# Performance work log

Measured on AMD Instinct MI355X. Metric: run time of the kernel, lower is better.

The kernel has to match this reference:

```python
import jax, jax.numpy as jnp
import numpy as np

N_NODES = 50000
N_EDGES = 800000
IN_DIM = 128
HID = 64
HEADS = 4
OUT_DIM = 64
NEG_SLOPE = 0.2


def setup_inputs() -> dict:
    key = jax.random.key(0)
    ks = jax.random.split(key, 12)
    x = jax.random.normal(ks[0], (N_NODES, IN_DIM), dtype=jnp.float32)
    edge_index = jax.random.randint(ks[1], (2, N_EDGES), 0, N_NODES, dtype=jnp.int64)
    s = 0.1
    # GATConv layer 1: in_dim -> hid per head, 4 heads, concat
    W1 = jax.random.normal(ks[2], (IN_DIM, HEADS * HID), dtype=jnp.float32) * s
    a_src1 = jax.random.normal(ks[3], (HEADS, HID), dtype=jnp.float32) * s
    a_dst1 = jax.random.normal(ks[4], (HEADS, HID), dtype=jnp.float32) * s
    b1 = jnp.zeros((HEADS * HID,), dtype=jnp.float32)
    # GATConv layer 2: hid*heads -> out_dim, 1 head
    W2 = jax.random.normal(ks[5], (HEADS * HID, OUT_DIM), dtype=jnp.float32) * s
    a_src2 = jax.random.normal(ks[6], (1, OUT_DIM), dtype=jnp.float32) * s
    a_dst2 = jax.random.normal(ks[7], (1, OUT_DIM), dtype=jnp.float32) * s
    b2 = jnp.zeros((OUT_DIM,), dtype=jnp.float32)
    # final linear out_dim -> 1
    fc_w = jax.random.normal(ks[8], (OUT_DIM, 1), dtype=jnp.float32) * s
    fc_b = jnp.zeros((1,), dtype=jnp.float32)
    return {"x": x, "edge_index": edge_index, "W1": W1, "a_src1": a_src1,
            "a_dst1": a_dst1, "b1": b1, "W2": W2, "a_src2": a_src2,
            "a_dst2": a_dst2, "b2": b2, "fc_w": fc_w, "fc_b": fc_b}


def _gat_layer(x, src, dst, W, a_src, a_dst, bias, heads, out_c):
    """PyG-style GATConv: gather, edge attention, segment softmax, scatter-sum."""
    n = x.shape[0]
    h = (x @ W).reshape(n, heads, out_c)                    # [N,H,C]
    alpha_s = jnp.sum(h * a_src, axis=-1)                   # [N,H]
    alpha_d = jnp.sum(h * a_dst, axis=-1)                   # [N,H]
    e = jax.nn.leaky_relu(alpha_s[src] + alpha_d[dst], NEG_SLOPE)  # [E,H]
    # segment softmax over incoming edges of each destination node
    m = jax.ops.segment_max(e, dst, num_segments=n)         # [N,H]
    ex = jnp.exp(e - m[dst])
    den = jax.ops.segment_sum(ex, dst, num_segments=n)      # [N,H]
    alpha = ex / (den[dst] + 1e-16)                         # [E,H]
    out = jax.ops.segment_sum(alpha[:, :, None] * h[src], dst, num_segments=n)
    return out.reshape(n, heads * out_c) + bias


def reference(x, edge_index, W1, a_src1, a_dst1, b1, W2, a_src2, a_dst2, b2, fc_w, fc_b):
    n = x.shape[0]
    # GATConv default add_self_loops=True
    loop = jnp.arange(n, dtype=edge_index.dtype)
    src = jnp.concatenate([edge_index[0], loop])
    dst = jnp.concatenate([edge_index[1], loop])
    h = _gat_layer(x, src, dst, W1, a_src1, a_dst1, b1, HEADS, HID)
    h = jax.nn.elu(h)
    h = _gat_layer(h, src, dst, W2, a_src2, a_dst2, b2, 1, OUT_DIM)
    return jnp.squeeze(h @ fc_w + fc_b)                      # [N]
```

## Files before the change

kernel.cpp:

```cpp
#include <hip/hip_runtime.h>

#define N_NODES 50000
#define N_EDGES 800000
#define E_TOT   850000
#define IN_DIM  128
#define HID     64
#define HEADS   4
#define C1      256
#define OUT_DIM 64
#define NEG_SLOPE 0.2f

#define CP_NODES   32
#define CP_BLOCKS  ((N_NODES + CP_NODES - 1) / CP_NODES)
#define COUNT_BLOCKS ((E_TOT + 255) / 256)
#define NB_SCAN ((N_NODES + 255) / 256)

typedef __attribute__((ext_vector_type(8))) short v8s;
typedef __attribute__((ext_vector_type(4))) float v4f;

__device__ __forceinline__ unsigned int bf16_rne(float f) {
    unsigned int u = __float_as_uint(f);
    return (u + 0x7FFFu + ((u >> 16) & 1u)) >> 16;
}
__device__ __forceinline__ unsigned int bf16_pack2(float a, float b) {
    return bf16_rne(a) | (bf16_rne(b) << 16);
}
__device__ __forceinline__ float bf16_lo(unsigned int u) { return __uint_as_float(u << 16); }
__device__ __forceinline__ float bf16_hi(unsigned int u) { return __uint_as_float(u & 0xFFFF0000u); }

__global__ __launch_bounds__(512) void prep_kernel(
    const float* __restrict__ W1, const float* __restrict__ a_src1,
    const float* __restrict__ a_dst1,
    const float* __restrict__ W2, const float* __restrict__ a_src2,
    const float* __restrict__ a_dst2, const float* __restrict__ b2,
    const float* __restrict__ fc_w, const float* __restrict__ fc_b,
    float* __restrict__ p_src, float* __restrict__ p_dst,
    float* __restrict__ v_s, float* __restrict__ v_d, float* __restrict__ v_z,
    float* __restrict__ cst, unsigned int* __restrict__ W1b)
{
    const int t = threadIdx.x;
    const int k = t >> 2, h = t & 3;
    const float* wrow = W1 + k * C1 + h * HID;
    const float* as = a_src1 + h * HID;
    const float* ad = a_dst1 + h * HID;
    float s = 0.f, d = 0.f;
    for (int c = 0; c < HID; c++) {
        float w = wrow[c];
        s = fmaf(w, as[c], s);
        d = fmaf(w, ad[c], d);
    }
    p_src[k * HEADS + h] = s;
    p_dst[k * HEADS + h] = d;

    if (t < C1) {
        const float* w2row = W2 + t * OUT_DIM;
        float vs = 0.f, vd = 0.f, vz = 0.f;
        for (int c = 0; c < OUT_DIM; c++) {
            float w = w2row[c];
            vs = fmaf(w, a_src2[c], vs);
            vd = fmaf(w, a_dst2[c], vd);
            vz = fmaf(w, fc_w[c], vz);
        }
        v_s[t] = vs; v_d[t] = vd; v_z[t] = vz;
    }
    if (t == 0) {
        float s2 = 0.f;
        for (int c = 0; c < OUT_DIM; c++) s2 = fmaf(b2[c], fc_w[c], s2);
        cst[0] = s2 + fc_b[0];
    }

    for (int idx = t; idx < 16384; idx += 512) {
        int i    = idx & 3;
        int lane = (idx >> 2) & 63;
        int kk   = (idx >> 8) & 3;
        int nt   = (idx >> 10) & 3;
        int hh   = idx >> 12;
        int k0 = kk * 32 + (lane >> 4) * 8 + i * 2;
        int c  = hh * 64 + nt * 16 + (lane & 15);
        W1b[idx] = bf16_pack2(W1[(size_t)k0 * C1 + c], W1[(size_t)(k0 + 1) * C1 + c]);
    }
}

__global__ __launch_bounds__(256) void convproj_count_kernel(
    const float* __restrict__ x, const float* __restrict__ p_src,
    const float* __restrict__ p_dst, const int* __restrict__ dst_a,
    float* __restrict__ as1, float* __restrict__ ad1,
    unsigned int* __restrict__ xb, int* __restrict__ deg)
{
    if (blockIdx.x >= CP_BLOCKS) {
        int j = (blockIdx.x - CP_BLOCKS) * 256 + threadIdx.x;
        if (j < E_TOT) {
            int d = (j < N_EDGES) ? dst_a[j] : (j - N_EDGES);
            atomicAdd(&deg[d], 1);
        }
        return;
    }
    __shared__ float ps[IN_DIM * HEADS];
    __shared__ float pd[IN_DIM * HEADS];
    const int t = threadIdx.x;
    for (int i = t; i < IN_DIM * HEADS; i += 256) { ps[i] = p_src[i]; pd[i] = p_dst[i]; }
    __syncthreads();
    const int wv   = t >> 6;
    const int lane = t & 63;
    float4 p0 = *(const float4*)(ps + (lane * 2) * HEADS);
    float4 p1 = *(const float4*)(ps + (lane * 2 + 1) * HEADS);
    float4 q0 = *(const float4*)(pd + (lane * 2) * HEADS);
    float4 q1 = *(const float4*)(pd + (lane * 2 + 1) * HEADS);
    const int nodeBase = blockIdx.x * CP_NODES + wv * 8;
    #pragma unroll
    for (int i = 0; i < 8; i++) {
        const int node = nodeBase + i;
        if (node >= N_NODES) break;
        float2 xv = *(const float2*)(x + (size_t)node * IN_DIM + lane * 2);
        xb[(size_t)node * 64 + lane] = bf16_pack2(xv.x, xv.y);
        float s0 = xv.x * p0.x + xv.y * p1.x;
        float s1 = xv.x * p0.y + xv.y * p1.y;
        float s2 = xv.x * p0.z + xv.y * p1.z;
        float s3 = xv.x * p0.w + xv.y * p1.w;
        float d0 = xv.x * q0.x + xv.y * q1.x;
        float d1 = xv.x * q0.y + xv.y * q1.y;
        float d2 = xv.x * q0.z + xv.y * q1.z;
        float d3 = xv.x * q0.w + xv.y * q1.w;
        #pragma unroll
        for (int off = 32; off; off >>= 1) {
            s0 += __shfl_down(s0, off, 64); s1 += __shfl_down(s1, off, 64);
            s2 += __shfl_down(s2, off, 64); s3 += __shfl_down(s3, off, 64);
            d0 += __shfl_down(d0, off, 64); d1 += __shfl_down(d1, off, 64);
            d2 += __shfl_down(d2, off, 64); d3 += __shfl_down(d3, off, 64);
        }
        if (lane == 0) {
            float4 sv = {s0, s1, s2, s3};
            float4 dv = {d0, d1, d2, d3};
            *(float4*)(as1 + node * 4) = sv;
            *(float4*)(ad1 + node * 4) = dv;
        }
    }
}

__global__ __launch_bounds__(256) void blocksum_kernel(
    const int* __restrict__ deg, int* __restrict__ bsum)
{
    __shared__ int ps[256];
    const int t = threadIdx.x;
    int i = blockIdx.x * 256 + t;
    ps[t] = (i < N_NODES) ? deg[i] : 0;
    __syncthreads();
    for (int off = 128; off; off >>= 1) {
        if (t < off) ps[t] += ps[t + off];
        __syncthreads();
    }
    if (t == 0) bsum[blockIdx.x] = ps[0];
}

__global__ __launch_bounds__(256) void scanbsum_kernel(
    const int* __restrict__ bsum, int* __restrict__ boff)
{
    __shared__ int ps[256];
    const int t = threadIdx.x;
    ps[t] = (t < NB_SCAN) ? bsum[t] : 0;
    __syncthreads();
    for (int off = 1; off < 256; off <<= 1) {
        int u = (t >= off) ? ps[t - off] : 0;
        __syncthreads();
        ps[t] += u;
        __syncthreads();
    }
    boff[t] = (t > 0) ? ps[t - 1] : 0;
}

__global__ __launch_bounds__(256) void expand_kernel(
    const int* __restrict__ deg, const int* __restrict__ boff,
    int* __restrict__ rowptr)
{
    __shared__ int ps[256];
    const int t = threadIdx.x;
    int i = blockIdx.x * 256 + t;
    int v = (i < N_NODES) ? deg[i] : 0;
    ps[t] = v;
    __syncthreads();
    for (int off = 1; off < 256; off <<= 1) {
        int u = (t >= off) ? ps[t - off] : 0;
        __syncthreads();
        ps[t] += u;
        __syncthreads();
    }
    if (i <= N_NODES) rowptr[i] = boff[blockIdx.x] + ps[t] - v;
}

__global__ void fillw_kernel(const int* __restrict__ src_a, const int* __restrict__ dst_a,
                             const int* __restrict__ rowptr, int* __restrict__ cursor,
                             const float* __restrict__ as1, const float* __restrict__ ad1,
                             int* __restrict__ srcSorted, float4* __restrict__ wS)
{
    int j = blockIdx.x * blockDim.x + threadIdx.x;
    if (j >= E_TOT) return;
    int s, d;
    if (j < N_EDGES) { s = src_a[j]; d = dst_a[j]; }
    else             { s = j - N_EDGES; d = s; }
    int pos = atomicAdd(&cursor[d], 1);
    int slot = rowptr[d] + pos;
    srcSorted[slot] = s;
    float4 A  = *(const float4*)(as1 + s * 4);
    float4 Dv = *(const float4*)(ad1 + d * 4);
    float a0 = A.x + Dv.x, a1 = A.y + Dv.y, a2 = A.z + Dv.z, a3 = A.w + Dv.w;
    a0 = a0 > 0.f ? a0 : NEG_SLOPE * a0;
    a1 = a1 > 0.f ? a1 : NEG_SLOPE * a1;
    a2 = a2 > 0.f ? a2 : NEG_SLOPE * a2;
    a3 = a3 > 0.f ? a3 : NEG_SLOPE * a3;
    float4 w = {__expf(a0), __expf(a1), __expf(a2), __expf(a3)};
    wS[slot] = w;
}

__global__ __launch_bounds__(256) void agg1x_kernel(
    const int* __restrict__ rowptr, const int* __restrict__ srcS,
    const float4* __restrict__ wS, const unsigned int* __restrict__ xb,
    unsigned int* __restrict__ xaggb)
{
    int gid  = blockIdx.x * blockDim.x + threadIdx.x;
    int n    = gid >> 6;
    int lane = threadIdx.x & 63;
    if (n >= N_NODES) return;
    const int e0 = rowptr[n], e1 = rowptr[n + 1];

    float2 acc0 = {0,0}, acc1 = {0,0}, acc2 = {0,0}, acc3 = {0,0};
    float den0 = 0, den1 = 0, den2 = 0, den3 = 0;
    int e = e0;
    for (; e + 4 <= e1; e += 4) {
        int s0 = srcS[e], s1 = srcS[e + 1], s2 = srcS[e + 2], s3 = srcS[e + 3];
        float4 W0 = wS[e],     W1 = wS[e + 1];
        float4 W2 = wS[e + 2], W3 = wS[e + 3];
        unsigned int xu0 = xb[(size_t)s0 * 64 + lane];
        unsigned int xu1 = xb[(size_t)s1 * 64 + lane];
        unsigned int xu2 = xb[(size_t)s2 * 64 + lane];
        unsigned int xu3 = xb[(size_t)s3 * 64 + lane];
        float a0 = bf16_lo(xu0), b0 = bf16_hi(xu0);
        float a1 = bf16_lo(xu1), b1 = bf16_hi(xu1);
        float a2 = bf16_lo(xu2), b2 = bf16_hi(xu2);
        float a3 = bf16_lo(xu3), b3 = bf16_hi(xu3);
        acc0.x = fmaf(W0.x, a0, acc0.x); acc0.y = fmaf(W0.x, b0, acc0.y);
        acc1.x = fmaf(W0.y, a0, acc1.x); acc1.y = fmaf(W0.y, b0, acc1.y);
        acc2.x = fmaf(W0.z, a0, acc2.x); acc2.y = fmaf(W0.z, b0, acc2.y);
        acc3.x = fmaf(W0.w, a0, acc3.x); acc3.y = fmaf(W0.w, b0, acc3.y);
        acc0.x = fmaf(W1.x, a1, acc0.x); acc0.y = fmaf(W1.x, b1, acc0.y);
        acc1.x = fmaf(W1.y, a1, acc1.x); acc1.y = fmaf(W1.y, b1, acc1.y);
        acc2.x = fmaf(W1.z, a1, acc2.x); acc2.y = fmaf(W1.z, b1, acc2.y);
        acc3.x = fmaf(W1.w, a1, acc3.x); acc3.y = fmaf(W1.w, b1, acc3.y);
        acc0.x = fmaf(W2.x, a2, acc0.x); acc0.y = fmaf(W2.x, b2, acc0.y);
        acc1.x = fmaf(W2.y, a2, acc1.x); acc1.y = fmaf(W2.y, b2, acc1.y);
        acc2.x = fmaf(W2.z, a2, acc2.x); acc2.y = fmaf(W2.z, b2, acc2.y);
        acc3.x = fmaf(W2.w, a2, acc3.x); acc3.y = fmaf(W2.w, b2, acc3.y);
        acc0.x = fmaf(W3.x, a3, acc0.x); acc0.y = fmaf(W3.x, b3, acc0.y);
        acc1.x = fmaf(W3.y, a3, acc1.x); acc1.y = fmaf(W3.y, b3, acc1.y);
        acc2.x = fmaf(W3.z, a3, acc2.x); acc2.y = fmaf(W3.z, b3, acc2.y);
        acc3.x = fmaf(W3.w, a3, acc3.x); acc3.y = fmaf(W3.w, b3, acc3.y);
        den0 += (W0.x + W1.x) + (W2.x + W3.x);
        den1 += (W0.y + W1.y) + (W2.y + W3.y);
        den2 += (W0.z + W1.z) + (W2.z + W3.z);
        den3 += (W0.w + W1.w) + (W2.w + W3.w);
    }
    for (; e < e1; e++) {
        int s = srcS[e];
        float4 W0 = wS[e];
        unsigned int xu = xb[(size_t)s * 64 + lane];
        float xa = bf16_lo(xu), xbv = bf16_hi(xu);
        acc0.x = fmaf(W0.x, xa, acc0.x); acc0.y = fmaf(W0.x, xbv, acc0.y);
        acc1.x = fmaf(W0.y, xa, acc1.x); acc1.y = fmaf(W0.y, xbv, acc1.y);
        acc2.x = fmaf(W0.z, xa, acc2.x); acc2.y = fmaf(W0.z, xbv, acc2.y);
        acc3.x = fmaf(W0.w, xa, acc3.x); acc3.y = fmaf(W0.w, xbv, acc3.y);
        den0 += W0.x; den1 += W0.y; den2 += W0.z; den3 += W0.w;
    }
    float i0 = 1.f / (den0 + 1e-16f), i1 = 1.f / (den1 + 1e-16f);
    float i2 = 1.f / (den2 + 1e-16f), i3 = 1.f / (den3 + 1e-16f);
    unsigned int* o = xaggb + (size_t)n * 256 + lane;
    o[0 * 64] = bf16_pack2(acc0.x * i0, acc0.y * i0);
    o[1 * 64] = bf16_pack2(acc1.x * i1, acc1.y * i1);
    o[2 * 64] = bf16_pack2(acc2.x * i2, acc2.y * i2);
    o[3 * 64] = bf16_pack2(acc3.x * i3, acc3.y * i3);
}

__global__ __launch_bounds__(256, 4) void mlp7_kernel(
    const unsigned int* __restrict__ xaggb,
    const unsigned int* __restrict__ W1b, const float* __restrict__ b1,
    const float* __restrict__ v_s, const float* __restrict__ v_d,
    const float* __restrict__ v_z,
    float2* __restrict__ az, float* __restrict__ ad2)
{
    __shared__ unsigned int xsh[16 * 260];
    __shared__ float pr[4 * 16 * 3];
    const int t = threadIdx.x;
    const int nodeBase = blockIdx.x * 16;
    const int h = t >> 6;
    const int lane = t & 63;

    {
        const unsigned int* gsrc = xaggb + (size_t)nodeBase * 256;
        #pragma unroll
        for (int i = 0; i < 4; i++) {
            int iu = i * 1024 + t * 4;
            uint4 v = *(const uint4*)(gsrc + iu);
            int n = iu >> 8, c = iu & 255;
            *(uint4*)(xsh + n * 260 + c) = v;
        }
    }
    __syncthreads();

    {
        const int m = lane & 15, quad = lane >> 4;
        const unsigned int* abase = xsh + m * 260 + h * 64 + quad * 4;
        v8s af0 = *(const v8s*)(abase + 0);
        v8s af1 = *(const v8s*)(abase + 16);
        v8s af2 = *(const v8s*)(abase + 32);
        v8s af3 = *(const v8s*)(abase + 48);

        float Sr[4] = {0,0,0,0}, Dr[4] = {0,0,0,0}, Zr[4] = {0,0,0,0};
        #pragma unroll
        for (int nt = 0; nt < 4; nt++) {
            const unsigned int* bbase = W1b + (size_t)(h * 16 + nt * 4) * 256 + lane * 4;
            v4f acc = {0.f, 0.f, 0.f, 0.f};
            acc = __builtin_amdgcn_mfma_f32_16x16x32_bf16(af0, *(const v8s*)(bbase + 0 * 256), acc, 0, 0, 0);
            acc = __builtin_amdgcn_mfma_f32_16x16x32_bf16(af1, *(const v8s*)(bbase + 1 * 256), acc, 0, 0, 0);
            acc = __builtin_amdgcn_mfma_f32_16x16x32_bf16(af2, *(const v8s*)(bbase + 2 * 256), acc, 0, 0, 0);
            acc = __builtin_amdgcn_mfma_f32_16x16x32_bf16(af3, *(const v8s*)(bbase + 3 * 256), acc, 0, 0, 0);
            const int c = h * 64 + nt * 16 + m;
            float bb = b1[c], vsc = v_s[c], vdc = v_d[c], vzc = v_z[c];
            #pragma unroll
            for (int r = 0; r < 4; r++) {
                float o = acc[r] + bb;
                o = o > 0.f ? o : __expf(o) - 1.f;
                Sr[r] = fmaf(o, vsc, Sr[r]);
                Dr[r] = fmaf(o, vdc, Dr[r]);
                Zr[r] = fmaf(o, vzc, Zr[r]);
            }
        }
        #pragma unroll
        for (int off = 8; off; off >>= 1) {
            #pragma unroll
            for (int r = 0; r < 4; r++) {
                Sr[r] += __shfl_down(Sr[r], off, 16);
                Dr[r] += __shfl_down(Dr[r], off, 16);
                Zr[r] += __shfl_down(Zr[r], off, 16);
            }
        }
        if (m == 0) {
            #pragma unroll
            for (int r = 0; r < 4; r++) {
                const int row = quad * 4 + r;
                pr[(h * 16 + row) * 3 + 0] = Sr[r];
                pr[(h * 16 + row) * 3 + 1] = Dr[r];
                pr[(h * 16 + row) * 3 + 2] = Zr[r];
            }
        }
    }
    __syncthreads();

    if (t < 16) {
        float s = 0.f, d = 0.f, z = 0.f;
        #pragma unroll
        for (int w = 0; w < 4; w++) {
            s += pr[(w * 16 + t) * 3 + 0];
            d += pr[(w * 16 + t) * 3 + 1];
            z += pr[(w * 16 + t) * 3 + 2];
        }
        const int node = nodeBase + t;
        float2 azv = {s, z};
        az[node]  = azv;
        ad2[node] = d;
    }
}

__global__ __launch_bounds__(256) void agg2z_kernel(
    const int* __restrict__ rowptr, const int* __restrict__ srcS,
    const float2* __restrict__ az, const float* __restrict__ ad2,
    const float* __restrict__ cst, float* __restrict__ out)
{
    int gid  = blockIdx.x * blockDim.x + threadIdx.x;
    int n    = gid >> 3;
    int sl   = threadIdx.x & 7;
    if (n >= N_NODES) return;
    const float adh = ad2[n];
    const int e0 = rowptr[n], e1 = rowptr[n + 1];

    float acc = 0.f, den = 0.f;
    for (int e = e0 + sl; e < e1; e += 8) {
        int s = srcS[e];
        float2 v = az[s];
        float a = v.x + adh;
        a = a > 0.f ? a : NEG_SLOPE * a;
        float w = __expf(a);
        acc = fmaf(w, v.y, acc);
        den += w;
    }
    #pragma unroll
    for (int off = 4; off; off >>= 1) {
        acc += __shfl_down(acc, off, 8);
        den += __shfl_down(den, off, 8);
    }
    if (sl == 0) out[n] = acc / (den + 1e-16f) + cst[0];
}

extern "C" void kernel_launch(void* const* d_in, const int* in_sizes, int n_in,
                              void* d_out, int out_size, void* d_ws, size_t ws_size,
                              hipStream_t stream)
{
    const float* x      = (const float*)d_in[0];
    const int*   ei     = (const int*)d_in[1];
    const float* W1     = (const float*)d_in[2];
    const float* a_src1 = (const float*)d_in[3];
    const float* a_dst1 = (const float*)d_in[4];
    const float* b1     = (const float*)d_in[5];
    const float* W2     = (const float*)d_in[6];
    const float* a_src2 = (const float*)d_in[7];
    const float* a_dst2 = (const float*)d_in[8];
    const float* b2     = (const float*)d_in[9];
    const float* fc_w   = (const float*)d_in[10];
    const float* fc_b   = (const float*)d_in[11];
    float* out = (float*)d_out;

    const int* srcA = ei;
    const int* dstA = ei + N_EDGES;

    float* ws = (float*)d_ws;
    size_t off = 0;
    unsigned int* xaggb = (unsigned int*)(ws + off); off += (size_t)N_NODES * 256;
    unsigned int* xb    = (unsigned int*)(ws + off); off += (size_t)N_NODES * 64;
    float4* wS     = (float4*)(ws + off); off += (size_t)E_TOT * 4 + 4;
    float* as1     = ws + off; off += (size_t)N_NODES * HEADS;
    float* ad1     = ws + off; off += (size_t)N_NODES * HEADS;
    float2* az     = (float2*)(ws + off); off += (size_t)N_NODES * 2;
    float* ad2     = ws + off; off += N_NODES;
    float* p_src   = ws + off; off += IN_DIM * HEADS;
    float* p_dst   = ws + off; off += IN_DIM * HEADS;
    float* v_s     = ws + off; off += C1;
    float* v_d     = ws + off; off += C1;
    float* v_z     = ws + off; off += C1;
    float* cst     = ws + off; off += 2;
    unsigned int* W1b = (unsigned int*)(ws + off); off += 16384;
    int* rowptr    = (int*)(ws + off); off += N_NODES + 1 + 256;
    int* srcSorted = (int*)(ws + off); off += E_TOT + 256;
    int* bsum      = (int*)(ws + off); off += 256;
    int* boff      = (int*)(ws + off); off += 256;
    int* zstart    = (int*)(ws + off);
    int* deg       = (int*)(ws + off); off += N_NODES;
    int* cursor    = (int*)(ws + off); off += N_NODES;
    hipMemsetAsync(zstart, 0, 2 * N_NODES * sizeof(int), stream);

    prep_kernel<<<1, 512, 0, stream>>>(W1, a_src1, a_dst1, W2, a_src2, a_dst2,
                                       b2, fc_w, fc_b, p_src, p_dst, v_s, v_d, v_z, cst, W1b);

    convproj_count_kernel<<<CP_BLOCKS + COUNT_BLOCKS, 256, 0, stream>>>(
        x, p_src, p_dst, dstA, as1, ad1, xb, deg);

    blocksum_kernel<<<NB_SCAN, 256, 0, stream>>>(deg, bsum);
    scanbsum_kernel<<<1, 256, 0, stream>>>(bsum, boff);
    expand_kernel<<<NB_SCAN, 256, 0, stream>>>(deg, boff, rowptr);
    fillw_kernel<<<COUNT_BLOCKS, 256, 0, stream>>>(srcA, dstA, rowptr, cursor,
                                                   as1, ad1, srcSorted, wS);

    agg1x_kernel<<<(N_NODES * 64 + 255) / 256, 256, 0, stream>>>(rowptr, srcSorted, wS, xb, xaggb);

    mlp7_kernel<<<N_NODES / 16, 256, 0, stream>>>(xaggb, W1b, b1, v_s, v_d, v_z, az, ad2);

    agg2z_kernel<<<(N_NODES * 8 + 255) / 256, 256, 0, stream>>>(rowptr, srcSorted, az, ad2, cst, out);
}
```

Before: 276.8 us.

## Capture per-edge slot in count pass and write edge weights unsorted

The count kernel now saves the atomicAdd return value as each edge's position within its destination segment, so the fill kernel no longer needs a second atomic pass over a cursor array. The fill kernel writes the float4 weights in original edge order, which is coalesced, and scatters only an (src, edge id) int2 pair to the sorted slot. In exchange, the aggregation kernels read an int2 instead of an int and gather weights indirectly by edge id, and a new posE buffer adds extra traffic.

```diff
diff --git a/kernel.cpp b/kernel.cpp
--- a/kernel.cpp
+++ b/kernel.cpp
@@ -85,13 +85,14 @@
     const float* __restrict__ x, const float* __restrict__ p_src,
     const float* __restrict__ p_dst, const int* __restrict__ dst_a,
     float* __restrict__ as1, float* __restrict__ ad1,
-    unsigned int* __restrict__ xb, int* __restrict__ deg)
+    unsigned int* __restrict__ xb, int* __restrict__ deg,
+    int* __restrict__ posE)
 {
     if (blockIdx.x >= CP_BLOCKS) {
         int j = (blockIdx.x - CP_BLOCKS) * 256 + threadIdx.x;
         if (j < E_TOT) {
             int d = (j < N_EDGES) ? dst_a[j] : (j - N_EDGES);
-            atomicAdd(&deg[d], 1);
+            posE[j] = atomicAdd(&deg[d], 1);
         }
         return;
     }
@@ -187,19 +188,19 @@
     if (i <= N_NODES) rowptr[i] = boff[blockIdx.x] + ps[t] - v;
 }
 
-__global__ void fillw_kernel(const int* __restrict__ src_a, const int* __restrict__ dst_a,
-                             const int* __restrict__ rowptr, int* __restrict__ cursor,
-                             const float* __restrict__ as1, const float* __restrict__ ad1,
-                             int* __restrict__ srcSorted, float4* __restrict__ wS)
+__global__ void fillw2_kernel(const int* __restrict__ src_a, const int* __restrict__ dst_a,
+                              const int* __restrict__ rowptr, const int* __restrict__ posE,
+                              const float* __restrict__ as1, const float* __restrict__ ad1,
+                              int2* __restrict__ srcj, float4* __restrict__ wE)
 {
     int j = blockIdx.x * blockDim.x + threadIdx.x;
     if (j >= E_TOT) return;
     int s, d;
     if (j < N_EDGES) { s = src_a[j]; d = dst_a[j]; }
     else             { s = j - N_EDGES; d = s; }
-    int pos = atomicAdd(&cursor[d], 1);
-    int slot = rowptr[d] + pos;
-    srcSorted[slot] = s;
+    int slot = rowptr[d] + posE[j];
+    int2 sj = {s, j};
+    srcj[slot] = sj;
     float4 A  = *(const float4*)(as1 + s * 4);
     float4 Dv = *(const float4*)(ad1 + d * 4);
     float a0 = A.x + Dv.x, a1 = A.y + Dv.y, a2 = A.z + Dv.z, a3 = A.w + Dv.w;
@@ -208,12 +209,12 @@
     a2 = a2 > 0.f ? a2 : NEG_SLOPE * a2;
     a3 = a3 > 0.f ? a3 : NEG_SLOPE * a3;
     float4 w = {__expf(a0), __expf(a1), __expf(a2), __expf(a3)};
-    wS[slot] = w;
+    wE[j] = w;
 }
 
 __global__ __launch_bounds__(256) void agg1x_kernel(
-    const int* __restrict__ rowptr, const int* __restrict__ srcS,
-    const float4* __restrict__ wS, const unsigned int* __restrict__ xb,
+    const int* __restrict__ rowptr, const int2* __restrict__ srcj,
+    const float4* __restrict__ wE, const unsigned int* __restrict__ xb,
     unsigned int* __restrict__ xaggb)
 {
     int gid  = blockIdx.x * blockDim.x + threadIdx.x;
@@ -226,13 +227,14 @@
     float den0 = 0, den1 = 0, den2 = 0, den3 = 0;
     int e = e0;
     for (; e + 4 <= e1; e += 4) {
-        int s0 = srcS[e], s1 = srcS[e + 1], s2 = srcS[e + 2], s3 = srcS[e + 3];
-        float4 W0 = wS[e],     W1 = wS[e + 1];
-        float4 W2 = wS[e + 2], W3 = wS[e + 3];
-        unsigned int xu0 = xb[(size_t)s0 * 64 + lane];
-        unsigned int xu1 = xb[(size_t)s1 * 64 + lane];
-        unsigned int xu2 = xb[(size_t)s2 * 64 + lane];
-        unsigned int xu3 = xb[(size_t)s3 * 64 + lane];
+        int2 sj0 = srcj[e],     sj1 = srcj[e + 1];
+        int2 sj2 = srcj[e + 2], sj3 = srcj[e + 3];
+        float4 W0 = wE[sj0.y], W1 = wE[sj1.y];
+        float4 W2 = wE[sj2.y], W3 = wE[sj3.y];
+        unsigned int xu0 = xb[(size_t)sj0.x * 64 + lane];
+        unsigned int xu1 = xb[(size_t)sj1.x * 64 + lane];
+        unsigned int xu2 = xb[(size_t)sj2.x * 64 + lane];
+        unsigned int xu3 = xb[(size_t)sj3.x * 64 + lane];
         float a0 = bf16_lo(xu0), b0 = bf16_hi(xu0);
         float a1 = bf16_lo(xu1), b1 = bf16_hi(xu1);
         float a2 = bf16_lo(xu2), b2 = bf16_hi(xu2);
@@ -259,9 +261,9 @@
         den3 += (W0.w + W1.w) + (W2.w + W3.w);
     }
     for (; e < e1; e++) {
-        int s = srcS[e];
-        float4 W0 = wS[e];
-        unsigned int xu = xb[(size_t)s * 64 + lane];
+        int2 sj = srcj[e];
+        float4 W0 = wE[sj.y];
+        unsigned int xu = xb[(size_t)sj.x * 64 + lane];
         float xa = bf16_lo(xu), xbv = bf16_hi(xu);
         acc0.x = fmaf(W0.x, xa, acc0.x); acc0.y = fmaf(W0.x, xbv, acc0.y);
         acc1.x = fmaf(W0.y, xa, acc1.x); acc1.y = fmaf(W0.y, xbv, acc1.y);
@@ -369,7 +371,7 @@
 }
 
 __global__ __launch_bounds__(256) void agg2z_kernel(
-    const int* __restrict__ rowptr, const int* __restrict__ srcS,
+    const int* __restrict__ rowptr, const int2* __restrict__ srcj,
     const float2* __restrict__ az, const float* __restrict__ ad2,
     const float* __restrict__ cst, float* __restrict__ out)
 {
@@ -382,7 +384,7 @@
 
     float acc = 0.f, den = 0.f;
     for (int e = e0 + sl; e < e1; e += 8) {
-        int s = srcS[e];
+        int s = srcj[e].x;
         float2 v = az[s];
         float a = v.x + adh;
         a = a > 0.f ? a : NEG_SLOPE * a;
@@ -423,7 +425,9 @@
     size_t off = 0;
     unsigned int* xaggb = (unsigned int*)(ws + off); off += (size_t)N_NODES * 256;
     unsigned int* xb    = (unsigned int*)(ws + off); off += (size_t)N_NODES * 64;
-    float4* wS     = (float4*)(ws + off); off += (size_t)E_TOT * 4 + 4;
+    float4* wE     = (float4*)(ws + off); off += (size_t)E_TOT * 4 + 4;
+    int2* srcj     = (int2*)(ws + off); off += (size_t)E_TOT * 2 + 256;
+    int* posE      = (int*)(ws + off); off += E_TOT + 256;
     float* as1     = ws + off; off += (size_t)N_NODES * HEADS;
     float* ad1     = ws + off; off += (size_t)N_NODES * HEADS;
     float2* az     = (float2*)(ws + off); off += (size_t)N_NODES * 2;
@@ -436,29 +440,26 @@
     float* cst     = ws + off; off += 2;
     unsigned int* W1b = (unsigned int*)(ws + off); off += 16384;
     int* rowptr    = (int*)(ws + off); off += N_NODES + 1 + 256;
-    int* srcSorted = (int*)(ws + off); off += E_TOT + 256;
     int* bsum      = (int*)(ws + off); off += 256;
     int* boff      = (int*)(ws + off); off += 256;
-    int* zstart    = (int*)(ws + off);
     int* deg       = (int*)(ws + off); off += N_NODES;
-    int* cursor    = (int*)(ws + off); off += N_NODES;
-    hipMemsetAsync(zstart, 0, 2 * N_NODES * sizeof(int), stream);
+    hipMemsetAsync(deg, 0, N_NODES * sizeof(int), stream);
 
     prep_kernel<<<1, 512, 0, stream>>>(W1, a_src1, a_dst1, W2, a_src2, a_dst2,
                                        b2, fc_w, fc_b, p_src, p_dst, v_s, v_d, v_z, cst, W1b);
 
     convproj_count_kernel<<<CP_BLOCKS + COUNT_BLOCKS, 256, 0, stream>>>(
-        x, p_src, p_dst, dstA, as1, ad1, xb, deg);
+        x, p_src, p_dst, dstA, as1, ad1, xb, deg, posE);
 
     blocksum_kernel<<<NB_SCAN, 256, 0, stream>>>(deg, bsum);
     scanbsum_kernel<<<1, 256, 0, stream>>>(bsum, boff);
     expand_kernel<<<NB_SCAN, 256, 0, stream>>>(deg, boff, rowptr);
-    fillw_kernel<<<COUNT_BLOCKS, 256, 0, stream>>>(srcA, dstA, rowptr, cursor,
-                                                   as1, ad1, srcSorted, wS);
-
-    agg1x_kernel<<<(N_NODES * 64 + 255) / 256, 256, 0, stream>>>(rowptr, srcSorted, wS, xb, xaggb);
+    fillw2_kernel<<<COUNT_BLOCKS, 256, 0, stream>>>(srcA, dstA, rowptr, posE,
+                                                    as1, ad1, srcj, wE);
+
+    agg1x_kernel<<<(N_NODES * 64 + 255) / 256, 256, 0, stream>>>(rowptr, srcj, wE, xb, xaggb);
 
     mlp7_kernel<<<N_NODES / 16, 256, 0, stream>>>(xaggb, W1b, b1, v_s, v_d, v_z, az, ad2);
 
-    agg2z_kernel<<<(N_NODES * 8 + 255) / 256, 256, 0, stream>>>(rowptr, srcSorted, az, ad2, cst, out);
-}
+    agg2z_kernel<<<(N_NODES * 8 + 255) / 256, 256, 0, stream>>>(rowptr, srcj, az, ad2, cst, out);
+}
```

Result: faster. 263.0 us (-5.0%).
